# Optimization experiments

Hardware: AMD Instinct MI355X
Metric: run time of the kernel (lower is better)

## Reference

```python
import jax, jax.numpy as jnp
import numpy as np

D_MODEL = 256; D_FLOW = 128; D_FFN = 1024
N_HEADS = 8; N_LEVELS = 3; N_POINTS = 4
D_HEAD = D_MODEL // N_HEADS
SHAPES = np.array([[128, 128], [64, 64], [32, 32]], dtype=np.int64)


def setup_inputs():
    key = jax.random.key(0)
    ks = jax.random.split(key, 12)
    N = 2
    LeNin = int((SHAPES[:, 0] * SHAPES[:, 1]).sum())
    Lq = int(SHAPES[0, 0] * SHAPES[0, 1])
    lsi = np.concatenate([[0], np.cumsum(SHAPES[:, 0] * SHAPES[:, 1])[:-1]])
    s = 0.02
    return {
        'src': jax.random.normal(ks[0], (N, LeNin, D_MODEL), jnp.float32),
        'flow': jax.random.normal(ks[1], (N, Lq, D_FLOW), jnp.float32),
        'spatial_shapes': jnp.asarray(SHAPES, jnp.int32),
        'level_start_index': jnp.asarray(lsi, jnp.int32),
        'w_value': jax.random.normal(ks[2], (D_MODEL, D_MODEL), jnp.float32) * s,
        'b_value': jnp.zeros((D_MODEL,), jnp.float32),
        'w_off': jax.random.normal(ks[3], (D_FLOW, N_HEADS * N_LEVELS * N_POINTS * 2), jnp.float32) * s,
        'b_off': jax.random.normal(ks[4], (N_HEADS * N_LEVELS * N_POINTS * 2,), jnp.float32) * 0.5,
        'w_attn': jax.random.normal(ks[5], (D_FLOW, N_HEADS * N_LEVELS * N_POINTS), jnp.float32) * s,
        'b_attn': jnp.zeros((N_HEADS * N_LEVELS * N_POINTS,), jnp.float32),
        'w_out': jax.random.normal(ks[6], (D_MODEL, D_MODEL), jnp.float32) * s,
        'b_out': jnp.zeros((D_MODEL,), jnp.float32),
        'gamma': jnp.ones((D_MODEL,), jnp.float32),
        'beta': jnp.zeros((D_MODEL,), jnp.float32),
        'w1': jax.random.normal(ks[7], (D_MODEL, D_FFN), jnp.float32) * s,
        'b1': jnp.zeros((D_FFN,), jnp.float32),
        'w2': jax.random.normal(ks[8], (D_FFN, D_MODEL), jnp.float32) * s,
        'b2': jnp.zeros((D_MODEL,), jnp.float32),
    }


def _bilinear_level(v, xy, H, W):
    # v: [N, nh, H*W, dh]; xy: [N, Lq, nh, np, 2] normalized to [0,1]
    # grid_sample(align_corners=False) semantics: pixel = loc * size - 0.5, zero padding
    N, Lq = xy.shape[0], xy.shape[1]
    x = xy[..., 0] * W - 0.5
    y = xy[..., 1] * H - 0.5
    x0 = jnp.floor(x); y0 = jnp.floor(y)
    dx = x - x0; dy = y - y0
    acc = jnp.zeros((N, N_HEADS, Lq * N_POINTS, v.shape[-1]), v.dtype)
    corners = ((x0, y0, (1 - dx) * (1 - dy)),
               (x0 + 1, y0, dx * (1 - dy)),
               (x0, y0 + 1, (1 - dx) * dy),
               (x0 + 1, y0 + 1, dx * dy))
    for ix, iy, w in corners:
        valid = (ix >= 0) & (ix <= W - 1) & (iy >= 0) & (iy <= H - 1)
        xi = jnp.clip(ix, 0, W - 1).astype(jnp.int32)
        yi = jnp.clip(iy, 0, H - 1).astype(jnp.int32)
        idx = (yi * W + xi).transpose(0, 2, 1, 3).reshape(N, N_HEADS, Lq * N_POINTS)
        g = jnp.take_along_axis(v, idx[..., None], axis=2)  # [N, nh, Lq*np, dh]
        wv = (w * valid).transpose(0, 2, 1, 3).reshape(N, N_HEADS, Lq * N_POINTS, 1)
        acc = acc + wv * g
    return acc


def reference(src, flow, spatial_shapes, level_start_index, w_value, b_value,
              w_off, b_off, w_attn, b_attn, w_out, b_out, gamma, beta, w1, b1, w2, b2):
    ss = np.asarray(jax.device_get(spatial_shapes))
    lsi = np.asarray(jax.device_get(level_start_index))
    N, LeNin, _ = src.shape
    Lq = flow.shape[1]
    value = (src @ w_value + b_value).reshape(N, LeNin, N_HEADS, D_HEAD)
    off = (flow @ w_off + b_off).reshape(N, Lq, N_HEADS, N_LEVELS, N_POINTS, 2)
    attn = jax.nn.softmax((flow @ w_attn + b_attn).reshape(N, Lq, N_HEADS, N_LEVELS * N_POINTS), axis=-1)
    attn = attn.reshape(N, Lq, N_HEADS, N_LEVELS, N_POINTS)
    # reference points on level-0 grid (valid_ratios == 1)
    H0, W0 = int(ss[0, 0]), int(ss[0, 1])
    ry, rx = jnp.meshgrid(jnp.linspace(0.5, H0 - 0.5, H0) / H0,
                          jnp.linspace(0.5, W0 - 0.5, W0) / W0, indexing='ij')
    ref = jnp.stack([rx.reshape(-1), ry.reshape(-1)], -1)  # [Lq, 2] (x, y)
    norm = jnp.asarray(np.stack([ss[:, 1], ss[:, 0]], -1), jnp.float32)  # [nl, 2] = (W, H)
    loc = ref[None, :, None, None, None, :] + off / norm[None, None, None, :, None, :]
    acc = jnp.zeros((N, Lq, N_HEADS, D_HEAD), src.dtype)
    for l in range(N_LEVELS):
        H, W = int(ss[l, 0]), int(ss[l, 1])
        st = int(lsi[l])
        v = value[:, st:st + H * W].transpose(0, 2, 1, 3)  # [N, nh, HW, dh]
        s_l = _bilinear_level(v, loc[:, :, :, l], H, W).reshape(N, N_HEADS, Lq, N_POINTS, D_HEAD)
        acc = acc + jnp.einsum('bhqpd,bqhp->bqhd', s_l, attn[:, :, :, l])
    src2 = acc.reshape(N, Lq, D_MODEL) @ w_out + b_out
    x = src2  # dropout is identity at inference
    mu = x.mean(-1, keepdims=True)
    var = ((x - mu) ** 2).mean(-1, keepdims=True)
    ln = (x - mu) / jnp.sqrt(var + 1e-5) * gamma + beta
    ffn = jax.nn.relu(ln @ w1 + b1) @ w2 + b2
    return x + ffn
```

## Files before the change

### kernel.cpp

```cpp
#include <hip/hip_runtime.h>
#include <cstdint>
#include <cstddef>

#define D_MODEL  256
#define D_FLOW   128
#define D_FFN    1024
#define N_HEADS  8
#define N_LEVELS 3
#define N_POINTS 4
#define D_HEAD   32
#define LQ       16384
#define LENIN    21504
#define NB       2

typedef unsigned short ushort;
typedef __attribute__((ext_vector_type(8))) short bf16x8;
typedef __attribute__((ext_vector_type(4))) float f32x4;

__device__ __forceinline__ ushort f2b(float f) {
    uint32_t u = __float_as_uint(f);
    uint32_t r = (u + 0x7fffu + ((u >> 16) & 1u)) >> 16;
    return (ushort)r;
}

__device__ __forceinline__ void gl_lds16(const void* g, void* l) {
    __builtin_amdgcn_global_load_lds(
        (const __attribute__((address_space(1))) unsigned int*)g,
        (__attribute__((address_space(3))) unsigned int*)l,
        16, 0, 0);
}

template<bool A_FP32, bool RELU, bool RESID, bool OUT_BF16>
__global__ __launch_bounds__(256)
void mfma_gemm(const void* __restrict__ Ain, const ushort* __restrict__ Bt,
               const float* __restrict__ bias, const float* __restrict__ resid,
               void* __restrict__ Cout, int N, int K)
{
    __shared__ ushort As[128 * 64];
    __shared__ ushort Bs[128 * 64];

    const int tid  = threadIdx.x;
    const int wave = tid >> 6;
    const int lane = tid & 63;
    const int quad = lane >> 4;
    const int l16  = lane & 15;
    const int wr   = (wave >> 1) * 64;
    const int wc   = (wave & 1) * 64;

    const int nx = gridDim.x;
    int lin = blockIdx.y * nx + blockIdx.x;
    const int total = nx * gridDim.y;
    if ((total & 7) == 0) lin = (lin & 7) * (total >> 3) + (lin >> 3);
    const int by = lin / nx;
    const int bx = lin - by * nx;
    const int bm = by * 128;
    const int bn = bx * 128;

    const int sr  = lane >> 3;
    const int sc  = lane & 7;
    const int gch = sc ^ sr;

    f32x4 acc[4][4] = {};
    const int swz = l16 & 7;

    for (int k0 = 0; k0 < K; k0 += 64) {
        __syncthreads();
        if (A_FP32) {
            const float* Af = (const float*)Ain;
#pragma unroll
            for (int i = 0; i < 4; ++i) {
                const int row = wave * 32 + i * 8 + sr;
                const float* p = Af + (size_t)(bm + row) * K + k0 + gch * 8;
                const float4 v0 = *(const float4*)(p);
                const float4 v1 = *(const float4*)(p + 4);
                bf16x8 pk;
                pk[0] = (short)f2b(v0.x); pk[1] = (short)f2b(v0.y);
                pk[2] = (short)f2b(v0.z); pk[3] = (short)f2b(v0.w);
                pk[4] = (short)f2b(v1.x); pk[5] = (short)f2b(v1.y);
                pk[6] = (short)f2b(v1.z); pk[7] = (short)f2b(v1.w);
                *(bf16x8*)&As[(size_t)row * 64 + sc * 8] = pk;
            }
        } else {
            const ushort* Ab = (const ushort*)Ain;
#pragma unroll
            for (int i = 0; i < 4; ++i) {
                const int row = wave * 32 + i * 8;
                gl_lds16(Ab + (size_t)(bm + row + sr) * K + k0 + gch * 8,
                         As + (size_t)row * 64);
            }
        }
#pragma unroll
        for (int i = 0; i < 4; ++i) {
            const int row = wave * 32 + i * 8;
            gl_lds16(Bt + (size_t)(bn + row + sr) * K + k0 + gch * 8,
                     Bs + (size_t)row * 64);
        }
        __syncthreads();

#pragma unroll
        for (int kk = 0; kk < 2; ++kk) {
            bf16x8 af[4], bfr[4];
#pragma unroll
            for (int mi = 0; mi < 4; ++mi) {
                const int p = (kk * 4 + quad) ^ swz;
                af[mi] = *(const bf16x8*)&As[(wr + mi * 16 + l16) * 64 + p * 8];
            }
#pragma unroll
            for (int ni = 0; ni < 4; ++ni) {
                const int p = (kk * 4 + quad) ^ swz;
                bfr[ni] = *(const bf16x8*)&Bs[(wc + ni * 16 + l16) * 64 + p * 8];
            }
#pragma unroll
            for (int mi = 0; mi < 4; ++mi)
#pragma unroll
                for (int ni = 0; ni < 4; ++ni)
                    acc[mi][ni] = __builtin_amdgcn_mfma_f32_16x16x32_bf16(
                        af[mi], bfr[ni], acc[mi][ni], 0, 0, 0);
        }
    }

#pragma unroll
    for (int mi = 0; mi < 4; ++mi) {
#pragma unroll
        for (int ni = 0; ni < 4; ++ni) {
            const int col = bn + wc + ni * 16 + l16;
            const float bb = bias[col];
#pragma unroll
            for (int r = 0; r < 4; ++r) {
                const int row = bm + wr + mi * 16 + quad * 4 + r;
                const size_t idx = (size_t)row * N + col;
                float c = acc[mi][ni][r] + bb;
                if (RELU)  c = fmaxf(c, 0.f);
                if (RESID) c += resid[idx];
                if (OUT_BF16) ((ushort*)Cout)[idx] = f2b(c);
                else          ((float*)Cout)[idx]  = c;
            }
        }
    }
}

__global__ __launch_bounds__(256)
void gemm_ln_k(const ushort* __restrict__ A, const ushort* __restrict__ Bt,
               const float* __restrict__ bias, const float* __restrict__ gamma,
               const float* __restrict__ beta,
               float* __restrict__ xout, ushort* __restrict__ lnout, int K)
{
    __shared__ ushort As[64 * 32];
    __shared__ ushort Bs[256 * 32];
    __shared__ float  sS[64][33];
    __shared__ float  sS2[64][33];
    __shared__ float  sMu[64], sRi[64];

    const int tid  = threadIdx.x;
    const int wave = tid >> 6;
    const int lane = tid & 63;
    const int quad = lane >> 4;
    const int l16  = lane & 15;
    const int wr   = (wave >> 1) * 32;
    const int wc   = (wave & 1) * 128;
    const int bm   = blockIdx.x * 64;

    const int sr  = lane >> 2;
    const int sc  = lane & 3;
    const int gch = sc ^ (sr & 3);

    f32x4 acc[2][8] = {};
    const int swz = l16 & 3;

    for (int k0 = 0; k0 < K; k0 += 32) {
        __syncthreads();
        gl_lds16(A + (size_t)(bm + wave * 16 + sr) * K + k0 + gch * 8,
                 As + wave * 16 * 32);
#pragma unroll
        for (int i = 0; i < 4; ++i) {
            const int row = wave * 64 + i * 16;
            gl_lds16(Bt + (size_t)(row + sr) * K + k0 + gch * 8,
                     Bs + (size_t)row * 32);
        }
        __syncthreads();

        bf16x8 af[2], bfr[8];
#pragma unroll
        for (int mi = 0; mi < 2; ++mi)
            af[mi] = *(const bf16x8*)&As[(wr + mi * 16 + l16) * 32 + ((quad ^ swz) << 3)];
#pragma unroll
        for (int ni = 0; ni < 8; ++ni)
            bfr[ni] = *(const bf16x8*)&Bs[(wc + ni * 16 + l16) * 32 + ((quad ^ swz) << 3)];
#pragma unroll
        for (int mi = 0; mi < 2; ++mi)
#pragma unroll
            for (int ni = 0; ni < 8; ++ni)
                acc[mi][ni] = __builtin_amdgcn_mfma_f32_16x16x32_bf16(
                    af[mi], bfr[ni], acc[mi][ni], 0, 0, 0);
    }

    float bias8[8], g8[8], b8[8];
#pragma unroll
    for (int ni = 0; ni < 8; ++ni) {
        const int col = wc + ni * 16 + l16;
        bias8[ni] = bias[col];
        g8[ni]    = gamma[col];
        b8[ni]    = beta[col];
    }

#pragma unroll
    for (int mi = 0; mi < 2; ++mi)
#pragma unroll
        for (int r = 0; r < 4; ++r) {
            float s = 0.f, s2 = 0.f;
#pragma unroll
            for (int ni = 0; ni < 8; ++ni) {
                const float c = acc[mi][ni][r] + bias8[ni];
                s += c; s2 += c * c;
            }
            const int row = wr + mi * 16 + quad * 4 + r;
            sS[row][(wave & 1) * 16 + l16]  = s;
            sS2[row][(wave & 1) * 16 + l16] = s2;
        }
    __syncthreads();

    if (tid < 64) {
        float s = 0.f, s2 = 0.f;
#pragma unroll
        for (int j = 0; j < 32; ++j) { s += sS[tid][j]; s2 += sS2[tid][j]; }
        const float mu  = s * (1.f / 256.f);
        const float var = s2 * (1.f / 256.f) - mu * mu;
        sMu[tid] = mu;
        sRi[tid] = rsqrtf(var + 1e-5f);
    }
    __syncthreads();

#pragma unroll
    for (int mi = 0; mi < 2; ++mi)
#pragma unroll
        for (int r = 0; r < 4; ++r) {
            const int lrow = wr + mi * 16 + quad * 4 + r;
            const int grow = bm + lrow;
            const float mu = sMu[lrow], ri = sRi[lrow];
#pragma unroll
            for (int ni = 0; ni < 8; ++ni) {
                const int col = wc + ni * 16 + l16;
                const float c = acc[mi][ni][r] + bias8[ni];
                xout[(size_t)grow * 256 + col]  = c;
                lnout[(size_t)grow * 256 + col] = f2b((c - mu) * ri * g8[ni] + b8[ni]);
            }
        }
}

__global__ __launch_bounds__(512, 2)
void ffn_fused_k(const ushort* __restrict__ ln, const ushort* __restrict__ w1T,
                 const ushort* __restrict__ w2C, const float* __restrict__ b1v,
                 const float* __restrict__ b2v, float* __restrict__ out)
{
    extern __shared__ ushort smem[];
    ushort* const w1s = smem;
    ushort* const w2s = smem + 16384;
    ushort* const hS  = smem + 32768;
    ushort* const lnS = smem;

    const int tid  = threadIdx.x;
    const int wave = tid >> 6;
    const int lane = tid & 63;
    const int quad = lane >> 4;
    const int l16  = lane & 15;
    const int bm   = blockIdx.x * 128;

    const int R0g1 = (wave >> 1) * 32;
    const int C0g1 = (wave & 1) * 32;
    const int M0   = (wave & 1) * 64;
    const int N0   = (wave >> 1) * 64;

#pragma unroll
    for (int i = 0; i < 8; ++i) {
        const int r0 = (wave * 8 + i) * 2;
        const int r  = r0 + (lane >> 5);
        gl_lds16(ln + (size_t)(bm + r) * 256 + (((lane & 31) ^ (r & 7)) << 3),
                 lnS + r0 * 256);
    }
    __syncthreads();

    bf16x8 afA[2][8];
#pragma unroll
    for (int mt = 0; mt < 2; ++mt)
#pragma unroll
        for (int kk = 0; kk < 8; ++kk) {
            const int row = R0g1 + mt * 16 + l16;
            afA[mt][kk] = *(const bf16x8*)
                &lnS[row * 256 + (((kk * 4 + quad) ^ (row & 7)) << 3)];
        }
    __syncthreads();

#pragma unroll
    for (int i = 0; i < 4; ++i) {
        const int r0 = (wave * 4 + i) * 2;
        const int r  = r0 + (lane >> 5);
        gl_lds16(w1T + (size_t)r * 256 + (((lane & 31) ^ (r & 7)) << 3),
                 w1s + r0 * 256);
    }
    __syncthreads();

    f32x4 acc2[4][4] = {};

#pragma unroll 1
    for (int c = 0; c < 16; ++c) {
        {
            const ushort* src = w2C + (size_t)c * 16384;
#pragma unroll
            for (int i = 0; i < 4; ++i) {
                const int r0 = (wave * 4 + i) * 8;
                const int r  = r0 + (lane >> 3);
                gl_lds16(src + (size_t)r * 64 + (((lane & 7) ^ (r & 7)) << 3),
                         w2s + r0 * 64);
            }
        }

        f32x4 acc1[2][2] = {};
#pragma unroll
        for (int kk = 0; kk < 8; ++kk) {
            bf16x8 wf[2];
#pragma unroll
            for (int nt = 0; nt < 2; ++nt) {
                const int n = C0g1 + nt * 16 + l16;
                wf[nt] = *(const bf16x8*)
                    &w1s[n * 256 + (((kk * 4 + quad) ^ (n & 7)) << 3)];
            }
#pragma unroll
            for (int mt = 0; mt < 2; ++mt)
#pragma unroll
                for (int nt = 0; nt < 2; ++nt)
                    acc1[mt][nt] = __builtin_amdgcn_mfma_f32_16x16x32_bf16(
                        wf[nt], afA[mt][kk], acc1[mt][nt], 0, 0, 0);
        }

        {
            float4 bb[2];
#pragma unroll
            for (int nt = 0; nt < 2; ++nt)
                bb[nt] = *(const float4*)&b1v[c * 64 + C0g1 + nt * 16 + quad * 4];
#pragma unroll
            for (int mt = 0; mt < 2; ++mt) {
                const int m = R0g1 + mt * 16 + l16;
#pragma unroll
                for (int nt = 0; nt < 2; ++nt) {
                    const int oct = (C0g1 >> 2) + nt * 4 + quad;
                    ushort4 pk;
                    pk.x = f2b(fmaxf(acc1[mt][nt][0] + bb[nt].x, 0.f));
                    pk.y = f2b(fmaxf(acc1[mt][nt][1] + bb[nt].y, 0.f));
                    pk.z = f2b(fmaxf(acc1[mt][nt][2] + bb[nt].z, 0.f));
                    pk.w = f2b(fmaxf(acc1[mt][nt][3] + bb[nt].w, 0.f));
                    *(ushort4*)&hS[m * 64 + ((oct ^ ((m & 7) << 1)) << 2)] = pk;
                }
            }
        }
        __syncthreads();

        if (c < 15) {
#pragma unroll
            for (int i = 0; i < 4; ++i) {
                const int r0 = (wave * 4 + i) * 2;
                const int r  = r0 + (lane >> 5);
                gl_lds16(w1T + (size_t)((c + 1) * 64 + r) * 256
                             + (((lane & 31) ^ (r & 7)) << 3),
                         w1s + r0 * 256);
            }
        }

#pragma unroll
        for (int kk = 0; kk < 2; ++kk) {
            const int g = kk * 4 + quad;
            bf16x8 hf[4], wf2[4];
#pragma unroll
            for (int mt = 0; mt < 4; ++mt) {
                const int m = M0 + mt * 16 + l16;
                hf[mt] = *(const bf16x8*)&hS[m * 64 + ((g ^ (m & 7)) << 3)];
            }
#pragma unroll
            for (int nt = 0; nt < 4; ++nt) {
                const int n = N0 + nt * 16 + l16;
                wf2[nt] = *(const bf16x8*)&w2s[n * 64 + ((g ^ (n & 7)) << 3)];
            }
#pragma unroll
            for (int mt = 0; mt < 4; ++mt)
#pragma unroll
                for (int nt = 0; nt < 4; ++nt)
                    acc2[mt][nt] = __builtin_amdgcn_mfma_f32_16x16x32_bf16(
                        wf2[nt], hf[mt], acc2[mt][nt], 0, 0, 0);
        }
        __syncthreads();
    }

#pragma unroll
    for (int mt = 0; mt < 4; ++mt) {
        const int row = bm + M0 + mt * 16 + l16;
#pragma unroll
        for (int nt = 0; nt < 4; ++nt) {
            const int col = N0 + nt * 16 + quad * 4;
            float4* p = (float4*)(out + (size_t)row * 256 + col);
            const float4 b4 = *(const float4*)&b2v[col];
            float4 v = *p;
            v.x = v.x + acc2[mt][nt][0] + b4.x;
            v.y = v.y + acc2[mt][nt][1] + b4.y;
            v.z = v.z + acc2[mt][nt][2] + b4.z;
            v.w = v.w + acc2[mt][nt][3] + b4.w;
            *p = v;
        }
    }
}

__device__ __forceinline__ void acc8(float* a, uint4 g, float w) {
    a[0] = fmaf(w, __uint_as_float(g.x << 16), a[0]);
    a[1] = fmaf(w, __uint_as_float(g.x), a[1]);
    a[2] = fmaf(w, __uint_as_float(g.y << 16), a[2]);
    a[3] = fmaf(w, __uint_as_float(g.y), a[3]);
    a[4] = fmaf(w, __uint_as_float(g.z << 16), a[4]);
    a[5] = fmaf(w, __uint_as_float(g.z), a[5]);
    a[6] = fmaf(w, __uint_as_float(g.w << 16), a[6]);
    a[7] = fmaf(w, __uint_as_float(g.w), a[7]);
}

__global__ __launch_bounds__(256)
void sample_k(const ushort* __restrict__ value, const ushort* __restrict__ projc,
              ushort* __restrict__ acc)
{
    __shared__ float sOff[8][192];
    __shared__ float sAttn[8][96];

    const int tid = threadIdx.x;
    const int bid = blockIdx.x;
    const int bq0 = (((bid & 7) << 9) | (bid >> 3)) << 3;

    for (int i = tid; i < 8 * 288; i += 256) {
        const int qw = i / 288, j = i - qw * 288;
        const float v = __uint_as_float((uint32_t)projc[(size_t)(bq0 + qw) * 384 + j] << 16);
        if (j < 192) sOff[qw][j] = v;
        else         sAttn[qw][j - 192] = v;
    }
    __syncthreads();

    if (tid < 64) {
        const int qw = tid >> 3, h = tid & 7;
        float* row = &sAttn[qw][h * 12];
        float m = row[0];
#pragma unroll
        for (int j = 1; j < 12; ++j) m = fmaxf(m, row[j]);
        float s = 0.f;
#pragma unroll
        for (int j = 0; j < 12; ++j) { const float e = __expf(row[j] - m); row[j] = e; s += e; }
        const float inv = 1.f / s;
#pragma unroll
        for (int j = 0; j < 12; ++j) row[j] *= inv;
    }
    __syncthreads();

    const int wave = tid >> 6, lane = tid & 63;
    const int qh = lane >> 5;
    const int h  = (lane >> 2) & 7;
    const int cg = lane & 3;
    const int qw = wave * 2 + qh;
    const int bq = bq0 + qw;
    const int n  = bq >> 14;
    const int q  = bq & 16383;

    const float qx = (float)(q & 127) + 0.5f;
    const float qy = (float)(q >> 7) + 0.5f;

    const int LSIc[3] = {0, 16384, 20480};

    float a[8] = {0.f, 0.f, 0.f, 0.f, 0.f, 0.f, 0.f, 0.f};
    const ushort* vbase = value + (size_t)n * LENIN * D_MODEL + h * D_HEAD + cg * 8;

#pragma unroll
    for (int l = 0; l < N_LEVELS; ++l) {
        const int   W     = 128 >> l;
        const int   SH    = 7 - l;
        const float scale = 1.f / (float)(1 << l);
        const float cx    = qx * scale - 0.5f;
        const float cy    = qy * scale - 0.5f;
        const ushort* vlev = vbase + ((size_t)LSIc[l] << 8);
#pragma unroll
        for (int p = 0; p < N_POINTS; ++p) {
            const int ob = (h * N_LEVELS + l) * (N_POINTS * 2) + p * 2;
            const float aw = sAttn[qw][h * 12 + l * 4 + p];
            const float x = cx + sOff[qw][ob];
            const float y = cy + sOff[qw][ob + 1];
            const float x0f = floorf(x), y0f = floorf(y);
            const int x0 = (int)x0f, y0 = (int)y0f;
            const float dx = x - x0f, dy = y - y0f;
            float wx1 = dx * aw, wx0 = aw - wx1;
            float wy1 = dy,      wy0 = 1.f - dy;
            if ((unsigned)x0       > (unsigned)(W - 1)) wx0 = 0.f;
            if ((unsigned)(x0 + 1) > (unsigned)(W - 1)) wx1 = 0.f;
            if ((unsigned)y0       > (unsigned)(W - 1)) wy0 = 0.f;
            if ((unsigned)(y0 + 1) > (unsigned)(W - 1)) wy1 = 0.f;
            const int xi0 = min(max(x0, 0), W - 1);
            const int xi1 = min(max(x0 + 1, 0), W - 1);
            const int yi0 = min(max(y0, 0), W - 1);
            const int yi1 = min(max(y0 + 1, 0), W - 1);
            const uint4 g00 = *(const uint4*)(vlev + ((size_t)((yi0 << SH) + xi0) << 8));
            const uint4 g01 = *(const uint4*)(vlev + ((size_t)((yi0 << SH) + xi1) << 8));
            const uint4 g10 = *(const uint4*)(vlev + ((size_t)((yi1 << SH) + xi0) << 8));
            const uint4 g11 = *(const uint4*)(vlev + ((size_t)((yi1 << SH) + xi1) << 8));
            acc8(a, g00, wx0 * wy0);
            acc8(a, g01, wx1 * wy0);
            acc8(a, g10, wx0 * wy1);
            acc8(a, g11, wx1 * wy1);
        }
    }

    const uint32_t o0 = (uint32_t)f2b(a[0]) | ((uint32_t)f2b(a[1]) << 16);
    const uint32_t o1 = (uint32_t)f2b(a[2]) | ((uint32_t)f2b(a[3]) << 16);
    const uint32_t o2 = (uint32_t)f2b(a[4]) | ((uint32_t)f2b(a[5]) << 16);
    const uint32_t o3 = (uint32_t)f2b(a[6]) | ((uint32_t)f2b(a[7]) << 16);
    const uint4 ov = {o0, o1, o2, o3};
    *(uint4*)(acc + (size_t)bq * D_MODEL + h * D_HEAD + cg * 8) = ov;
}

__global__ __launch_bounds__(256)
void prep_all_k(const float* __restrict__ w_value, const float* __restrict__ w_out,
                const float* __restrict__ w1, const float* __restrict__ w2,
                const float* __restrict__ w_off, const float* __restrict__ b_off,
                const float* __restrict__ w_attn, const float* __restrict__ b_attn,
                ushort* __restrict__ wvT, ushort* __restrict__ woT,
                ushort* __restrict__ w1T, ushort* __restrict__ w2C,
                ushort* __restrict__ wcT, float* __restrict__ biasc)
{
    int i = blockIdx.x * 256 + threadIdx.x;
    if (i < 65536) {
        const int k = i >> 8, n = i & 255;
        wvT[(size_t)n * 256 + k] = f2b(w_value[i]);
        return;
    }
    i -= 65536;
    if (i < 65536) {
        const int k = i >> 8, n = i & 255;
        woT[(size_t)n * 256 + k] = f2b(w_out[i]);
        return;
    }
    i -= 65536;
    if (i < 262144) {
        const int k = i >> 10, n = i & 1023;
        w1T[(size_t)n * 256 + k] = f2b(w1[i]);
        return;
    }
    i -= 262144;
    if (i < 262144) {
        const int k = i >> 8, n = i & 255;
        w2C[(size_t)(k >> 6) * 16384 + n * 64 + (k & 63)] = f2b(w2[i]);
        return;
    }
    i -= 262144;
    if (i < 49152) {
        const int nn = i >> 7, k = i & 127;
        float v = 0.f;
        if (nn < 192)      v = w_off[(size_t)k * 192 + nn];
        else if (nn < 288) v = w_attn[(size_t)k * 96 + (nn - 192)];
        wcT[i] = f2b(v);
        return;
    }
    i -= 49152;
    if (i < 384) {
        float b = 0.f;
        if (i < 192)      b = b_off[i];
        else if (i < 288) b = b_attn[i - 192];
        biasc[i] = b;
    }
}

extern "C" void kernel_launch(void* const* d_in, const int* in_sizes, int n_in,
                              void* d_out, int out_size, void* d_ws, size_t ws_size,
                              hipStream_t stream)
{
    const float* src     = (const float*)d_in[0];
    const float* flow    = (const float*)d_in[1];
    const float* w_value = (const float*)d_in[4];
    const float* b_value = (const float*)d_in[5];
    const float* w_off   = (const float*)d_in[6];
    const float* b_off   = (const float*)d_in[7];
    const float* w_attn  = (const float*)d_in[8];
    const float* b_attn  = (const float*)d_in[9];
    const float* w_out   = (const float*)d_in[10];
    const float* b_out   = (const float*)d_in[11];
    const float* gamma   = (const float*)d_in[12];
    const float* beta    = (const float*)d_in[13];
    const float* w1      = (const float*)d_in[14];
    const float* b1      = (const float*)d_in[15];
    const float* w2      = (const float*)d_in[16];
    const float* b2      = (const float*)d_in[17];
    float* out = (float*)d_out;
    char*  wsb = (char*)d_ws;

    ushort* value_bf = (ushort*)(wsb);
    ushort* acc_bf   = (ushort*)(wsb + 22020096);
    ushort* projc_bf = (ushort*)(wsb + 67108864);
    ushort* ln_bf    = (ushort*)(wsb + 67108864);
    ushort* wvT      = (ushort*)(wsb + 92274688);
    ushort* woT      = (ushort*)(wsb + 92405760);
    ushort* w1T      = (ushort*)(wsb + 92536832);
    ushort* w2C      = (ushort*)(wsb + 93061120);
    ushort* wcT      = (ushort*)(wsb + 93585408);
    float*  biasc    = (float*) (wsb + 93683712);

    const int Mq = NB * LQ;
    const int Mv = NB * LENIN;

    static bool ffn_attr_done = false;
    if (!ffn_attr_done) {
        hipFuncSetAttribute((const void*)ffn_fused_k,
                            hipFuncAttributeMaxDynamicSharedMemorySize, 81920);
        ffn_attr_done = true;
    }

    prep_all_k<<<2754, 256, 0, stream>>>(w_value, w_out, w1, w2,
                                         w_off, b_off, w_attn, b_attn,
                                         wvT, woT, w1T, w2C, wcT, biasc);

    mfma_gemm<true, false, false, true><<<dim3(2, Mv / 128), 256, 0, stream>>>(
        src, wvT, b_value, nullptr, value_bf, 256, 256);

    mfma_gemm<true, false, false, true><<<dim3(3, Mq / 128), 256, 0, stream>>>(
        flow, wcT, biasc, nullptr, projc_bf, 384, 128);

    sample_k<<<Mq / 8, 256, 0, stream>>>(value_bf, projc_bf, acc_bf);

    gemm_ln_k<<<Mq / 64, 256, 0, stream>>>(
        acc_bf, woT, b_out, gamma, beta, out, ln_bf, 256);

    ffn_fused_k<<<Mq / 128, 512, 81920, stream>>>(ln_bf, w1T, w2C, b1, b2, out);
}
```

Measured before the change: 268.7 us.

## Software-pipeline fused FFN with double-buffered W1/H and register-loaded W2

Restructures the fused FFN loop so the second GEMM for chunk c-1 runs while chunk c's first GEMM proceeds. W1 tiles and hidden activations are double-buffered in LDS, which removes one barrier per iteration. W2 is re-laid out during prep so its fragments can be loaded straight from global memory into registers instead of staged through LDS. The LN input is also read directly from global memory into registers. This raises LDS use to 96KB per block, which may allow only one block per CU, and adds global-load latency for the W2 fragments.

After: 269.8 us. About the same (+0.4%).

```diff
diff --git a/kernel.cpp b/kernel.cpp
--- a/kernel.cpp
+++ b/kernel.cpp
@@ -249,14 +249,14 @@
 
 __global__ __launch_bounds__(512, 2)
 void ffn_fused_k(const ushort* __restrict__ ln, const ushort* __restrict__ w1T,
-                 const ushort* __restrict__ w2C, const float* __restrict__ b1v,
+                 const ushort* __restrict__ w2R, const float* __restrict__ b1v,
                  const float* __restrict__ b2v, float* __restrict__ out)
 {
     extern __shared__ ushort smem[];
-    ushort* const w1s = smem;
-    ushort* const w2s = smem + 16384;
-    ushort* const hS  = smem + 32768;
-    ushort* const lnS = smem;
+    ushort* const w1s0 = smem;
+    ushort* const w1s1 = smem + 16384;
+    ushort* const hs0  = smem + 32768;
+    ushort* const hs1  = smem + 40960;
 
     const int tid  = threadIdx.x;
     const int wave = tid >> 6;
@@ -270,32 +270,20 @@
     const int M0   = (wave & 1) * 64;
     const int N0   = (wave >> 1) * 64;
 
-#pragma unroll
-    for (int i = 0; i < 8; ++i) {
-        const int r0 = (wave * 8 + i) * 2;
-        const int r  = r0 + (lane >> 5);
-        gl_lds16(ln + (size_t)(bm + r) * 256 + (((lane & 31) ^ (r & 7)) << 3),
-                 lnS + r0 * 256);
-    }
-    __syncthreads();
-
     bf16x8 afA[2][8];
 #pragma unroll
     for (int mt = 0; mt < 2; ++mt)
 #pragma unroll
         for (int kk = 0; kk < 8; ++kk) {
-            const int row = R0g1 + mt * 16 + l16;
-            afA[mt][kk] = *(const bf16x8*)
-                &lnS[row * 256 + (((kk * 4 + quad) ^ (row & 7)) << 3)];
-        }
-    __syncthreads();
-
+            const int row = bm + R0g1 + mt * 16 + l16;
+            afA[mt][kk] = *(const bf16x8*)&ln[(size_t)row * 256 + (kk * 4 + quad) * 8];
+        }
 #pragma unroll
     for (int i = 0; i < 4; ++i) {
         const int r0 = (wave * 4 + i) * 2;
         const int r  = r0 + (lane >> 5);
         gl_lds16(w1T + (size_t)r * 256 + (((lane & 31) ^ (r & 7)) << 3),
-                 w1s + r0 * 256);
+                 w1s0 + r0 * 256);
     }
     __syncthreads();
 
@@ -303,14 +291,33 @@
 
 #pragma unroll 1
     for (int c = 0; c < 16; ++c) {
-        {
-            const ushort* src = w2C + (size_t)c * 16384;
+        ushort* const w1cur = (c & 1) ? w1s1 : w1s0;
+        ushort* const w1nxt = (c & 1) ? w1s0 : w1s1;
+        ushort* const hcur  = (c & 1) ? hs1  : hs0;
+        ushort* const hprv  = (c & 1) ? hs0  : hs1;
+
+        if (c < 15) {
 #pragma unroll
             for (int i = 0; i < 4; ++i) {
-                const int r0 = (wave * 4 + i) * 8;
-                const int r  = r0 + (lane >> 3);
-                gl_lds16(src + (size_t)r * 64 + (((lane & 7) ^ (r & 7)) << 3),
-                         w2s + r0 * 64);
+                const int r0 = (wave * 4 + i) * 2;
+                const int r  = r0 + (lane >> 5);
+                gl_lds16(w1T + (size_t)((c + 1) * 64 + r) * 256
+                             + (((lane & 31) ^ (r & 7)) << 3),
+                         w1nxt + r0 * 256);
+            }
+        }
+
+        bf16x8 w2f[2][4];
+        if (c >= 1) {
+#pragma unroll
+            for (int kk = 0; kk < 2; ++kk) {
+                const int g = kk * 4 + quad;
+                const ushort* base = w2R + ((size_t)((c - 1) * 8 + g)) * 2048;
+#pragma unroll
+                for (int nt = 0; nt < 4; ++nt) {
+                    const int n = N0 + nt * 16 + l16;
+                    w2f[kk][nt] = *(const bf16x8*)(base + n * 8);
+                }
             }
         }
 
@@ -322,7 +329,7 @@
             for (int nt = 0; nt < 2; ++nt) {
                 const int n = C0g1 + nt * 16 + l16;
                 wf[nt] = *(const bf16x8*)
-                    &w1s[n * 256 + (((kk * 4 + quad) ^ (n & 7)) << 3)];
+                    &w1cur[n * 256 + (((kk * 4 + quad) ^ (n & 7)) << 3)];
             }
 #pragma unroll
             for (int mt = 0; mt < 2; ++mt)
@@ -348,45 +355,60 @@
                     pk.y = f2b(fmaxf(acc1[mt][nt][1] + bb[nt].y, 0.f));
                     pk.z = f2b(fmaxf(acc1[mt][nt][2] + bb[nt].z, 0.f));
                     pk.w = f2b(fmaxf(acc1[mt][nt][3] + bb[nt].w, 0.f));
-                    *(ushort4*)&hS[m * 64 + ((oct ^ ((m & 7) << 1)) << 2)] = pk;
+                    *(ushort4*)&hcur[m * 64 + ((oct ^ ((m & 7) << 1)) << 2)] = pk;
                 }
             }
         }
+
+        if (c >= 1) {
+#pragma unroll
+            for (int kk = 0; kk < 2; ++kk) {
+                const int g = kk * 4 + quad;
+                bf16x8 hf[4];
+#pragma unroll
+                for (int mt = 0; mt < 4; ++mt) {
+                    const int m = M0 + mt * 16 + l16;
+                    hf[mt] = *(const bf16x8*)&hprv[m * 64 + ((g ^ (m & 7)) << 3)];
+                }
+#pragma unroll
+                for (int mt = 0; mt < 4; ++mt)
+#pragma unroll
+                    for (int nt = 0; nt < 4; ++nt)
+                        acc2[mt][nt] = __builtin_amdgcn_mfma_f32_16x16x32_bf16(
+                            w2f[kk][nt], hf[mt], acc2[mt][nt], 0, 0, 0);
+            }
+        }
         __syncthreads();
-
-        if (c < 15) {
-#pragma unroll
-            for (int i = 0; i < 4; ++i) {
-                const int r0 = (wave * 4 + i) * 2;
-                const int r  = r0 + (lane >> 5);
-                gl_lds16(w1T + (size_t)((c + 1) * 64 + r) * 256
-                             + (((lane & 31) ^ (r & 7)) << 3),
-                         w1s + r0 * 256);
-            }
-        }
-
+    }
+
+    {
+        bf16x8 w2f[2][4];
 #pragma unroll
         for (int kk = 0; kk < 2; ++kk) {
             const int g = kk * 4 + quad;
-            bf16x8 hf[4], wf2[4];
+            const ushort* base = w2R + ((size_t)(15 * 8 + g)) * 2048;
+#pragma unroll
+            for (int nt = 0; nt < 4; ++nt) {
+                const int n = N0 + nt * 16 + l16;
+                w2f[kk][nt] = *(const bf16x8*)(base + n * 8);
+            }
+        }
+#pragma unroll
+        for (int kk = 0; kk < 2; ++kk) {
+            const int g = kk * 4 + quad;
+            bf16x8 hf[4];
 #pragma unroll
             for (int mt = 0; mt < 4; ++mt) {
                 const int m = M0 + mt * 16 + l16;
-                hf[mt] = *(const bf16x8*)&hS[m * 64 + ((g ^ (m & 7)) << 3)];
-            }
-#pragma unroll
-            for (int nt = 0; nt < 4; ++nt) {
-                const int n = N0 + nt * 16 + l16;
-                wf2[nt] = *(const bf16x8*)&w2s[n * 64 + ((g ^ (n & 7)) << 3)];
+                hf[mt] = *(const bf16x8*)&hs1[m * 64 + ((g ^ (m & 7)) << 3)];
             }
 #pragma unroll
             for (int mt = 0; mt < 4; ++mt)
 #pragma unroll
                 for (int nt = 0; nt < 4; ++nt)
                     acc2[mt][nt] = __builtin_amdgcn_mfma_f32_16x16x32_bf16(
-                        wf2[nt], hf[mt], acc2[mt][nt], 0, 0, 0);
-        }
-        __syncthreads();
+                        w2f[kk][nt], hf[mt], acc2[mt][nt], 0, 0, 0);
+        }
     }
 
 #pragma unroll
@@ -521,7 +543,7 @@
                 const float* __restrict__ w_off, const float* __restrict__ b_off,
                 const float* __restrict__ w_attn, const float* __restrict__ b_attn,
                 ushort* __restrict__ wvT, ushort* __restrict__ woT,
-                ushort* __restrict__ w1T, ushort* __restrict__ w2C,
+                ushort* __restrict__ w1T, ushort* __restrict__ w2R,
                 ushort* __restrict__ wcT, float* __restrict__ biasc)
 {
     int i = blockIdx.x * 256 + threadIdx.x;
@@ -545,7 +567,7 @@
     i -= 262144;
     if (i < 262144) {
         const int k = i >> 8, n = i & 255;
-        w2C[(size_t)(k >> 6) * 16384 + n * 64 + (k & 63)] = f2b(w2[i]);
+        w2R[(size_t)(k >> 3) * 2048 + n * 8 + (k & 7)] = f2b(w2[i]);
         return;
     }
     i -= 262144;
@@ -596,7 +618,7 @@
     ushort* wvT      = (ushort*)(wsb + 92274688);
     ushort* woT      = (ushort*)(wsb + 92405760);
     ushort* w1T      = (ushort*)(wsb + 92536832);
-    ushort* w2C      = (ushort*)(wsb + 93061120);
+    ushort* w2R      = (ushort*)(wsb + 93061120);
     ushort* wcT      = (ushort*)(wsb + 93585408);
     float*  biasc    = (float*) (wsb + 93683712);
 
@@ -606,13 +628,13 @@
     static bool ffn_attr_done = false;
     if (!ffn_attr_done) {
         hipFuncSetAttribute((const void*)ffn_fused_k,
-                            hipFuncAttributeMaxDynamicSharedMemorySize, 81920);
+                            hipFuncAttributeMaxDynamicSharedMemorySize, 98304);
         ffn_attr_done = true;
     }
 
     prep_all_k<<<2754, 256, 0, stream>>>(w_value, w_out, w1, w2,
                                          w_off, b_off, w_attn, b_attn,
-                                         wvT, woT, w1T, w2C, wcT, biasc);
+                                         wvT, woT, w1T, w2R, wcT, biasc);
 
     mfma_gemm<true, false, false, true><<<dim3(2, Mv / 128), 256, 0, stream>>>(
         src, wvT, b_value, nullptr, value_bf, 256, 256);
@@ -625,5 +647,5 @@
     gemm_ln_k<<<Mq / 64, 256, 0, stream>>>(
         acc_bf, woT, b_out, gamma, beta, out, ln_bf, 256);
 
-    ffn_fused_k<<<Mq / 128, 512, 81920, stream>>>(ln_bf, w1T, w2C, b1, b2, out);
-}
+    ffn_fused_k<<<Mq / 128, 512, 98304, stream>>>(ln_bf, w1T, w2R, b1, b2, out);
+}
```
